# Kernel optimization log

Measured on AMD Instinct MI355X. Metric: run time of the kernel, lower is better.

The kernel has to match this reference:

```python
import jax, jax.numpy as jnp
import numpy as np

B, H, S, D = 4, 16, 1024, 64
MAX_REL = 128
VOCAB = 2 * MAX_REL + 1  # relative-position vocabulary


def setup_inputs() -> dict:
    key = jax.random.key(0)
    k1, k2, k3, k4 = jax.random.split(key, 4)
    tensor = jax.random.normal(k1, (B, H, S, D), dtype=jnp.float32)
    rel_keys_emb = jax.random.normal(k2, (VOCAB, D), dtype=jnp.float32) * 0.02
    rel_values_emb = jax.random.normal(k3, (VOCAB, D), dtype=jnp.float32) * 0.02
    # nn.Parameter initialized xavier_uniform_ on shape (1, H, 1, 1)
    bias = jax.random.uniform(k4, (1, H, 1, 1), dtype=jnp.float32, minval=-1.0, maxval=1.0)
    return {
        "tensor": tensor,
        "rel_keys_emb": rel_keys_emb,
        "rel_values_emb": rel_values_emb,
        "bias": bias,
        "max_relative_position": MAX_REL,
    }


def reference(tensor, rel_keys_emb, rel_values_emb, bias, max_relative_position):
    # forward(tensor, is_key=True, transpose=False)
    seq_len = tensor.shape[2]
    r = jnp.arange(seq_len)
    dist = jnp.clip(r[None, :] - r[:, None], -max_relative_position, max_relative_position)
    idx = dist + max_relative_position          # [S, S] in [0, 2*max_rel]
    rel_emb = rel_keys_emb[idx]                 # [S, S, D] gathered table
    # original: [S, B*H, D] @ [S, D, S] -> [S, B*H, S] -> [B, H, S, S]
    scores = jnp.einsum('bhsd,std->bhst', tensor, rel_emb)
    return scores + bias
```

## Files before the change

### kernel.cpp

```cpp
#include <hip/hip_runtime.h>


constexpr int S_   = 1024;
constexpr int D_   = 64;
constexpr int BQ   = 64;
constexpr int CPAD = 264;

typedef __attribute__((ext_vector_type(8))) short short8;
typedef __attribute__((ext_vector_type(4))) float f32x4;

__device__ __forceinline__ unsigned short f2bf(float x) {
  unsigned u = __float_as_uint(x);
  return (unsigned short)((u + 0x7fffu + ((u >> 16) & 1u)) >> 16);
}
__device__ __forceinline__ float bfu2f(unsigned short h) {
  return __uint_as_float(((unsigned)h) << 16);
}
__device__ __forceinline__ short8 pack8(float4 a, float4 b) {
  short8 r;
  r[0] = (short)f2bf(a.x); r[1] = (short)f2bf(a.y);
  r[2] = (short)f2bf(a.z); r[3] = (short)f2bf(a.w);
  r[4] = (short)f2bf(b.x); r[5] = (short)f2bf(b.y);
  r[6] = (short)f2bf(b.z); r[7] = (short)f2bf(b.w);
  return r;
}

__global__ __launch_bounds__(256, 4)
void relpos_v3(const float* __restrict__ tensor,
               const float* __restrict__ relk,
               const float* __restrict__ bias,
               float* __restrict__ out) {
  __shared__ __align__(16) unsigned short c_lds[4 * 16 * CPAD];

  const int tid  = threadIdx.x;
  const int lane = tid & 63;
  const int w    = tid >> 6;
  const int bh   = blockIdx.x >> 4;
  const int s0   = (blockIdx.x & 15) * BQ;
  const int h    = bh & 15;
  const int l15  = lane & 15;
  const int l4   = lane >> 4;

  unsigned short* cw = c_lds + w * 16 * CPAD;

  const float* xrow = tensor + ((size_t)(bh * S_ + s0 + 16 * w + l15)) * D_ + l4 * 8;
  short8 a0 = pack8(*reinterpret_cast<const float4*>(xrow),
                    *reinterpret_cast<const float4*>(xrow + 4));
  short8 a1 = pack8(*reinterpret_cast<const float4*>(xrow + 32),
                    *reinterpret_cast<const float4*>(xrow + 36));
  const float bv = bias[h];

  for (int nt = 0; nt < 17; ++nt) {
    const int vcol = 16 * nt + l15;
    const int erow = vcol > 256 ? 256 : vcol;
    const float* ep = relk + (size_t)erow * D_ + l4 * 8;
    short8 b0 = pack8(*reinterpret_cast<const float4*>(ep),
                      *reinterpret_cast<const float4*>(ep + 4));
    short8 b1 = pack8(*reinterpret_cast<const float4*>(ep + 32),
                      *reinterpret_cast<const float4*>(ep + 36));
    f32x4 acc = {0.f, 0.f, 0.f, 0.f};
    acc = __builtin_amdgcn_mfma_f32_16x16x32_bf16(a0, b0, acc, 0, 0, 0);
    acc = __builtin_amdgcn_mfma_f32_16x16x32_bf16(a1, b1, acc, 0, 0, 0);
    if (vcol <= 256) {
      const int r0 = l4 * 4;
#pragma unroll
      for (int i = 0; i < 4; ++i) {
        cw[(r0 + i) * CPAD + i + vcol] = f2bf(acc[i] + bv);
      }
    }
  }

#pragma unroll 4
  for (int rl = 0; rl < 16; ++rl) {
    const int s   = s0 + 16 * w + rl;
    const int pad = rl & 3;
    const unsigned short* cr = cw + rl * CPAD;
    float* orow = out + ((size_t)bh * S_ + s) * (size_t)S_;

    const float c0f   = bfu2f(cr[pad]);
    const float c256f = bfu2f(cr[pad + 256]);
    const float4 c0v   = make_float4(c0f, c0f, c0f, c0f);
    const float4 c256v = make_float4(c256f, c256f, c256f, c256f);

    const int w0  = s - 128 < 0 ? 0 : s - 128;
    const int w1  = s + 129 > S_ ? S_ : s + 129;
    const int La  = w0 & ~3;
    const int w0a = (w0 + 3) & ~3;
    const int w1a = w1 & ~3;
    const int Ra  = (w1 + 3) & ~3;

    const int nL = La >> 2;
    for (int j = 0; 64 * j < nL; ++j) {
      int slot = lane + 64 * j;
      if (slot < nL)
        *reinterpret_cast<float4*>(&orow[4 * slot]) = c0v;
    }
    const int nR = (S_ - Ra) >> 2;
    for (int j = 0; 64 * j < nR; ++j) {
      int slot = lane + 64 * j;
      if (slot < nR)
        *reinterpret_cast<float4*>(&orow[Ra + 4 * slot]) = c256v;
    }
    const int n4 = (w1a - w0a) >> 2;
    for (int j = 0; j < 2; ++j) {
      int slot = lane + 64 * j;
      if (slot < n4) {
        int t0 = w0a + 4 * slot;
        int vI = t0 - s + 128 + pad;
        uint2 q = *reinterpret_cast<const uint2*>(&cr[vI]);
        float4 o;
        o.x = __uint_as_float(q.x << 16);
        o.y = __uint_as_float(q.x & 0xffff0000u);
        o.z = __uint_as_float(q.y << 16);
        o.w = __uint_as_float(q.y & 0xffff0000u);
        *reinterpret_cast<float4*>(&orow[t0]) = o;
      }
    }
    if (lane < 8) {
      const bool left  = (w0 & 3) != 0;
      const bool right = (w1 & 3) != 0;
      const bool act   = (lane < 4) ? left : right;
      if (act) {
        int t = (lane < 4) ? (La + lane) : (w1a + (lane - 4));
        int v = t - s + 128;
        v = v < 0 ? 0 : (v > 256 ? 256 : v);
        orow[t] = bfu2f(cr[pad + v]);
      }
    }
  }
}

extern "C" void kernel_launch(void* const* d_in, const int* in_sizes, int n_in,
                              void* d_out, int out_size, void* d_ws, size_t ws_size,
                              hipStream_t stream) {
  const float* tensor = (const float*)d_in[0];
  const float* relk   = (const float*)d_in[1];
  const float* bias   = (const float*)d_in[3];
  float* out          = (float*)d_out;

  const int B = 4, H = 16;
  dim3 grid(B * H * (S_ / BQ));
  dim3 block(256);
  relpos_v3<<<grid, block, 0, stream>>>(tensor, relk, bias, out);
}
```

Baseline: 79.41 us.

## Pad LDS score rows with clamp values and write output in flat block-wide stream

Each row's 257 relative scores are now stored in a shared LDS buffer padded on both sides with the clamped edge values. The whole 256-thread block then writes the 64x1024 output tile as one contiguous stream of float4 stores, using a single clamped LDS index per store. This replaces the per-wave, per-row loops that had separate left-fill, window, right-fill and scalar edge paths. The cost is a block-wide barrier and extra padding stores into LDS.

```diff
diff --git a/kernel.cpp b/kernel.cpp
--- a/kernel.cpp
+++ b/kernel.cpp
@@ -1,10 +1,10 @@
 #include <hip/hip_runtime.h>
 
 
-constexpr int S_   = 1024;
-constexpr int D_   = 64;
-constexpr int BQ   = 64;
-constexpr int CPAD = 264;
+constexpr int S_     = 1024;
+constexpr int D_     = 64;
+constexpr int BQ     = 64;
+constexpr int CPITCH = 276;
 
 typedef __attribute__((ext_vector_type(8))) short short8;
 typedef __attribute__((ext_vector_type(4))) float f32x4;
@@ -12,9 +12,6 @@
 __device__ __forceinline__ unsigned short f2bf(float x) {
   unsigned u = __float_as_uint(x);
   return (unsigned short)((u + 0x7fffu + ((u >> 16) & 1u)) >> 16);
-}
-__device__ __forceinline__ float bfu2f(unsigned short h) {
-  return __uint_as_float(((unsigned)h) << 16);
 }
 __device__ __forceinline__ short8 pack8(float4 a, float4 b) {
   short8 r;
@@ -26,11 +23,11 @@
 }
 
 __global__ __launch_bounds__(256, 4)
-void relpos_v3(const float* __restrict__ tensor,
+void relpos_v4(const float* __restrict__ tensor,
                const float* __restrict__ relk,
                const float* __restrict__ bias,
                float* __restrict__ out) {
-  __shared__ __align__(16) unsigned short c_lds[4 * 16 * CPAD];
+  __shared__ __align__(16) unsigned short c_lds[BQ * CPITCH];
 
   const int tid  = threadIdx.x;
   const int lane = tid & 63;
@@ -40,8 +37,7 @@
   const int h    = bh & 15;
   const int l15  = lane & 15;
   const int l4   = lane >> 4;
-
-  unsigned short* cw = c_lds + w * 16 * CPAD;
+  const int r0   = 16 * w + l4 * 4;
 
   const float* xrow = tensor + ((size_t)(bh * S_ + s0 + 16 * w + l15)) * D_ + l4 * 8;
   short8 a0 = pack8(*reinterpret_cast<const float4*>(xrow),
@@ -50,6 +46,7 @@
                     *reinterpret_cast<const float4*>(xrow + 36));
   const float bv = bias[h];
 
+#pragma unroll 2
   for (int nt = 0; nt < 17; ++nt) {
     const int vcol = 16 * nt + l15;
     const int erow = vcol > 256 ? 256 : vcol;
@@ -62,71 +59,44 @@
     acc = __builtin_amdgcn_mfma_f32_16x16x32_bf16(a0, b0, acc, 0, 0, 0);
     acc = __builtin_amdgcn_mfma_f32_16x16x32_bf16(a1, b1, acc, 0, 0, 0);
     if (vcol <= 256) {
-      const int r0 = l4 * 4;
 #pragma unroll
       for (int i = 0; i < 4; ++i) {
-        cw[(r0 + i) * CPAD + i + vcol] = f2bf(acc[i] + bv);
+        c_lds[(r0 + i) * CPITCH + i + 4 + vcol] = f2bf(acc[i] + bv);
+      }
+    }
+    if (l15 == 0 && nt == 0) {
+#pragma unroll
+      for (int i = 0; i < 4; ++i) {
+        const unsigned short cv = f2bf(acc[i] + bv);
+        for (int j = 0; j <= i + 3; ++j) c_lds[(r0 + i) * CPITCH + j] = cv;
+      }
+    }
+    if (l15 == 0 && nt == 16) {
+#pragma unroll
+      for (int i = 0; i < 4; ++i) {
+        const unsigned short cv = f2bf(acc[i] + bv);
+        for (int j = i + 261; j < 268; ++j) c_lds[(r0 + i) * CPITCH + j] = cv;
       }
     }
   }
+  __syncthreads();
 
+  float* obase = out + ((size_t)bh * S_ + s0) * (size_t)S_;
+  const int mc = 132 - s0;
 #pragma unroll 4
-  for (int rl = 0; rl < 16; ++rl) {
-    const int s   = s0 + 16 * w + rl;
-    const int pad = rl & 3;
-    const unsigned short* cr = cw + rl * CPAD;
-    float* orow = out + ((size_t)bh * S_ + s) * (size_t)S_;
-
-    const float c0f   = bfu2f(cr[pad]);
-    const float c256f = bfu2f(cr[pad + 256]);
-    const float4 c0v   = make_float4(c0f, c0f, c0f, c0f);
-    const float4 c256v = make_float4(c256f, c256f, c256f, c256f);
-
-    const int w0  = s - 128 < 0 ? 0 : s - 128;
-    const int w1  = s + 129 > S_ ? S_ : s + 129;
-    const int La  = w0 & ~3;
-    const int w0a = (w0 + 3) & ~3;
-    const int w1a = w1 & ~3;
-    const int Ra  = (w1 + 3) & ~3;
-
-    const int nL = La >> 2;
-    for (int j = 0; 64 * j < nL; ++j) {
-      int slot = lane + 64 * j;
-      if (slot < nL)
-        *reinterpret_cast<float4*>(&orow[4 * slot]) = c0v;
-    }
-    const int nR = (S_ - Ra) >> 2;
-    for (int j = 0; 64 * j < nR; ++j) {
-      int slot = lane + 64 * j;
-      if (slot < nR)
-        *reinterpret_cast<float4*>(&orow[Ra + 4 * slot]) = c256v;
-    }
-    const int n4 = (w1a - w0a) >> 2;
-    for (int j = 0; j < 2; ++j) {
-      int slot = lane + 64 * j;
-      if (slot < n4) {
-        int t0 = w0a + 4 * slot;
-        int vI = t0 - s + 128 + pad;
-        uint2 q = *reinterpret_cast<const uint2*>(&cr[vI]);
-        float4 o;
-        o.x = __uint_as_float(q.x << 16);
-        o.y = __uint_as_float(q.x & 0xffff0000u);
-        o.z = __uint_as_float(q.y << 16);
-        o.w = __uint_as_float(q.y & 0xffff0000u);
-        *reinterpret_cast<float4*>(&orow[t0]) = o;
-      }
-    }
-    if (lane < 8) {
-      const bool left  = (w0 & 3) != 0;
-      const bool right = (w1 & 3) != 0;
-      const bool act   = (lane < 4) ? left : right;
-      if (act) {
-        int t = (lane < 4) ? (La + lane) : (w1a + (lane - 4));
-        int v = t - s + 128;
-        v = v < 0 ? 0 : (v > 256 ? 256 : v);
-        orow[t] = bfu2f(cr[pad + v]);
-      }
-    }
+  for (int it = 0; it < 64; ++it) {
+    const int idx = it * 256 + tid;
+    const int rl  = idx >> 8;
+    const int t0  = (idx & 255) << 2;
+    int m0 = t0 + (rl & 3) + mc - rl;
+    m0 = m0 < 0 ? 0 : (m0 > 264 ? 264 : m0);
+    const uint2 q = *reinterpret_cast<const uint2*>(&c_lds[rl * CPITCH + m0]);
+    float4 o;
+    o.x = __uint_as_float(q.x << 16);
+    o.y = __uint_as_float(q.x & 0xffff0000u);
+    o.z = __uint_as_float(q.y << 16);
+    o.w = __uint_as_float(q.y & 0xffff0000u);
+    *reinterpret_cast<float4*>(&obase[(size_t)idx * 4]) = o;
   }
 }
 
@@ -141,5 +111,5 @@
   const int B = 4, H = 16;
   dim3 grid(B * H * (S_ / BQ));
   dim3 block(256);
-  relpos_v3<<<grid, block, 0, stream>>>(tensor, relk, bias, out);
+  relpos_v4<<<grid, block, 0, stream>>>(tensor, relk, bias, out);
 }
```

Result: faster. 73.66 us (-7.2%).
